# Optimization experiments

Measured on AMD Instinct MI355X. Metric: run time of the kernel, lower is better.

Reference implementation:

```python
import jax, jax.numpy as jnp
import numpy as np

LOCAL_MAX_DISP = 12
STRIDE = 1


def setup_inputs() -> dict:
    key = jax.random.key(0)
    k1, k2 = jax.random.split(key)
    B, H, W, C = 8, 256, 512, 32
    feat_l = jax.random.normal(k1, (B, H, W, C), dtype=jnp.float32)
    feat_r = jax.random.normal(k2, (B, H, W, C), dtype=jnp.float32)
    return {"feat_l": feat_l, "feat_r": feat_r}


def reference(feat_l, feat_r):
    # Faithful translation of CostVolume2D.call:
    # For disparity i = d*stride:
    #   cost[:, :, w, d] = sum_c |feat_l[:, :, w, c] - feat_r[:, :, w-i, c]|  for w >= i
    #   cost[:, :, w, d] = sum_c |feat_l[:, :, w, c]|                         for w <  i
    # The w < i case equals L1(feat_l - 0), so zero-padding feat_r on the left
    # by i columns reproduces both branches in one fused abs-diff reduction.
    B, H, W, C = feat_l.shape
    n_disp = LOCAL_MAX_DISP // STRIDE  # 12

    def cost_at(i):
        # shift feat_r right by i columns, zero-fill on the left  -> [B, H, W, C]
        shifted_r = jnp.pad(feat_r, ((0, 0), (0, 0), (i, 0), (0, 0)))[:, :, :W, :]
        return jnp.sum(jnp.abs(feat_l - shifted_r), axis=-1)  # [B, H, W]

    # small fixed loop over disparities (n_disp = 12), vectorized over B,H,W,C
    cost = jnp.stack([cost_at(d * STRIDE) for d in range(n_disp)], axis=-1)
    return cost  # [B, H, W, n_disp]
```

## Files before the change

### kernel.cpp

```cpp
#include <hip/hip_runtime.h>


constexpr int Wd   = 512;
constexpr int ND   = 12;
constexpr int NCOL = 272;

typedef float vfloat4 __attribute__((ext_vector_type(4)));

__device__ __forceinline__ float l1_4(float4 a, float4 b) {
    return fabsf(a.x - b.x) + fabsf(a.y - b.y) + fabsf(a.z - b.z) + fabsf(a.w - b.w);
}

__global__ __launch_bounds__(256) void cost_volume_kernel(
    const float* __restrict__ fl,
    const float* __restrict__ fr,
    float* __restrict__ out)
{
    __shared__ float4 lds4[4 * NCOL];

    const int t    = threadIdx.x;
    const int wave = t >> 6;
    const int lane = t & 63;
    const int wstart = (blockIdx.x & 1) * 256;
    const int bh     = blockIdx.x >> 1;
    const float* fr_row = fr + (size_t)bh * Wd * 32;

    const int w = wstart + t;
    const size_t pix = (size_t)bh * Wd + w;
    const float4* lp = reinterpret_cast<const float4*>(fl) + pix * 8;

    float res[ND];
    #pragma unroll
    for (int d = 0; d < ND; ++d) res[d] = 0.f;
    float lsum = 0.f;

    #pragma unroll
    for (int h = 0; h < 2; ++h) {
        if (h == 1) __syncthreads();

        #pragma unroll
        for (int run = 0; run < 5; ++run) {
            const int colr = run * 64 + lane;
            int col = wstart - 11 + colr;
            col = max(col, 0);
            if (run < 4 || lane < 267 - 256) {
                __builtin_amdgcn_global_load_lds(
                    (const __attribute__((address_space(1))) void*)(fr_row + (size_t)col * 32 + (h * 4 + wave) * 4),
                    (__attribute__((address_space(3))) void*)(lds4 + wave * NCOL + colr),
                    16, 0, 0);
            }
        }

        float4 L[4];
        #pragma unroll
        for (int ql = 0; ql < 4; ++ql) {
            L[ql] = lp[h * 4 + ql];
            lsum += fabsf(L[ql].x) + fabsf(L[ql].y) + fabsf(L[ql].z) + fabsf(L[ql].w);
        }

        __syncthreads();

        #pragma unroll
        for (int ql = 0; ql < 4; ++ql) {
            const float4 Lq = L[ql];
            const float4* base = &lds4[ql * NCOL + t];
            #pragma unroll
            for (int d = 0; d < ND; ++d) {
                res[d] += l1_4(Lq, base[11 - d]);
            }
        }
    }

    #pragma unroll
    for (int d = 0; d < ND; ++d)
        if (w < d) res[d] = lsum;

    vfloat4* op = reinterpret_cast<vfloat4*>(out + pix * ND);
    vfloat4 o0 = {res[0], res[1], res[2],  res[3]};
    vfloat4 o1 = {res[4], res[5], res[6],  res[7]};
    vfloat4 o2 = {res[8], res[9], res[10], res[11]};
    __builtin_nontemporal_store(o0, op + 0);
    __builtin_nontemporal_store(o1, op + 1);
    __builtin_nontemporal_store(o2, op + 2);
}

extern "C" void kernel_launch(void* const* d_in, const int* in_sizes, int n_in,
                              void* d_out, int out_size, void* d_ws, size_t ws_size,
                              hipStream_t stream)
{
    const float* fl = (const float*)d_in[0];
    const float* fr = (const float*)d_in[1];
    float* out = (float*)d_out;

    const int grid = 8 * 256 * 2;
    cost_volume_kernel<<<grid, 256, 0, stream>>>(fl, fr, out);
}
```

Baseline: 66.24 us.

## Compute two adjacent pixels per thread with double-buffered LDS staging over channel passes

Each block now covers a full image row and each thread computes two neighbouring pixels, so one LDS read of a right-feature vector serves disparities for both pixels (13 reads instead of 24 per channel group). Right features are staged into a double-buffered LDS ring with an even/odd interleaved slot layout across four channel passes, and the async load of the next pass overlaps compute on the current one. This is meant to cut LDS read traffic and hide global-load latency. In exchange it halves the grid and the number of waves, and raises register pressure with two accumulator sets.

Measured after the change: 190.7 us. 2.88x slower.

```diff
diff --git a/kernel.cpp b/kernel.cpp
--- a/kernel.cpp
+++ b/kernel.cpp
@@ -1,14 +1,18 @@
 #include <hip/hip_runtime.h>
 
 
-constexpr int Wd   = 512;
-constexpr int ND   = 12;
-constexpr int NCOL = 272;
+constexpr int Wd    = 512;
+constexpr int ND    = 12;
+constexpr int NSLOT = 576;
+constexpr int NPASS = 4;
 
 typedef float vfloat4 __attribute__((ext_vector_type(4)));
 
 __device__ __forceinline__ float l1_4(float4 a, float4 b) {
     return fabsf(a.x - b.x) + fabsf(a.y - b.y) + fabsf(a.z - b.z) + fabsf(a.w - b.w);
+}
+__device__ __forceinline__ float abs4(float4 a) {
+    return fabsf(a.x) + fabsf(a.y) + fabsf(a.z) + fabsf(a.w);
 }
 
 __global__ __launch_bounds__(256) void cost_volume_kernel(
@@ -16,72 +20,89 @@
     const float* __restrict__ fr,
     float* __restrict__ out)
 {
-    __shared__ float4 lds4[4 * NCOL];
+    __shared__ float4 lds4[2][2 * NSLOT];
 
     const int t    = threadIdx.x;
     const int wave = t >> 6;
     const int lane = t & 63;
-    const int wstart = (blockIdx.x & 1) * 256;
-    const int bh     = blockIdx.x >> 1;
+    const int bh   = blockIdx.x;
     const float* fr_row = fr + (size_t)bh * Wd * 32;
+    const size_t pix0 = (size_t)bh * Wd + 2 * t;
+    const float4* lp = reinterpret_cast<const float4*>(fl);
 
-    const int w = wstart + t;
-    const size_t pix = (size_t)bh * Wd + w;
-    const float4* lp = reinterpret_cast<const float4*>(fl) + pix * 8;
+    int basen[7];
+    #pragma unroll
+    for (int m = 0; m < 7; ++m) {
+        const int n = t + m;
+        basen[m] = ((n >> 5) << 6) + (n & 31);
+    }
 
-    float res[ND];
-    #pragma unroll
-    for (int d = 0; d < ND; ++d) res[d] = 0.f;
-    float lsum = 0.f;
-
-    #pragma unroll
-    for (int h = 0; h < 2; ++h) {
-        if (h == 1) __syncthreads();
-
+    auto stage = [&](int pp, int buf) {
         #pragma unroll
-        for (int run = 0; run < 5; ++run) {
-            const int colr = run * 64 + lane;
-            int col = wstart - 11 + colr;
-            col = max(col, 0);
-            if (run < 4 || lane < 267 - 256) {
+        for (int j = 0; j < 5; ++j) {
+            const int i = wave + 4 * j;
+            if (i < 18) {
+                const int k = i >> 1, q = i & 1;
+                int col = 64 * k + 2 * (lane & 31) + (lane >> 5) - 11;
+                col = min(max(col, 0), Wd - 1);
                 __builtin_amdgcn_global_load_lds(
-                    (const __attribute__((address_space(1))) void*)(fr_row + (size_t)col * 32 + (h * 4 + wave) * 4),
-                    (__attribute__((address_space(3))) void*)(lds4 + wave * NCOL + colr),
+                    (const __attribute__((address_space(1))) void*)(fr_row + (size_t)col * 32 + (pp * 2 + q) * 4),
+                    (__attribute__((address_space(3))) void*)(&lds4[buf][q * NSLOT + 64 * k + lane]),
                     16, 0, 0);
             }
         }
+    };
 
-        float4 L[4];
+    float res0[ND], res1[ND];
+    #pragma unroll
+    for (int d = 0; d < ND; ++d) { res0[d] = 0.f; res1[d] = 0.f; }
+    float lsum0 = 0.f, lsum1 = 0.f;
+
+    stage(0, 0);
+
+    #pragma unroll
+    for (int pp = 0; pp < NPASS; ++pp) {
+        __syncthreads();
+        if (pp + 1 < NPASS) stage(pp + 1, (pp + 1) & 1);
+
+        const int buf = pp & 1;
         #pragma unroll
-        for (int ql = 0; ql < 4; ++ql) {
-            L[ql] = lp[h * 4 + ql];
-            lsum += fabsf(L[ql].x) + fabsf(L[ql].y) + fabsf(L[ql].z) + fabsf(L[ql].w);
-        }
-
-        __syncthreads();
-
-        #pragma unroll
-        for (int ql = 0; ql < 4; ++ql) {
-            const float4 Lq = L[ql];
-            const float4* base = &lds4[ql * NCOL + t];
+        for (int q = 0; q < 2; ++q) {
+            const float4 A0 = lp[pix0 * 8 + pp * 2 + q];
+            const float4 A1 = lp[(pix0 + 1) * 8 + pp * 2 + q];
+            lsum0 += abs4(A0);
+            lsum1 += abs4(A1);
+            const float4* plane = &lds4[buf][q * NSLOT];
             #pragma unroll
-            for (int d = 0; d < ND; ++d) {
-                res[d] += l1_4(Lq, base[11 - d]);
+            for (int E = 0; E <= 12; ++E) {
+                const float4 rv = plane[basen[E >> 1] + 32 * (E & 1)];
+                if (E <= 11) res0[11 - E] += l1_4(A0, rv);
+                if (E >= 1)  res1[12 - E] += l1_4(A1, rv);
             }
         }
     }
 
-    #pragma unroll
-    for (int d = 0; d < ND; ++d)
-        if (w < d) res[d] = lsum;
+    if (t < 6) {
+        #pragma unroll
+        for (int d = 0; d < ND; ++d) {
+            if (d > 2 * t)     res0[d] = lsum0;
+            if (d > 2 * t + 1) res1[d] = lsum1;
+        }
+    }
 
-    vfloat4* op = reinterpret_cast<vfloat4*>(out + pix * ND);
-    vfloat4 o0 = {res[0], res[1], res[2],  res[3]};
-    vfloat4 o1 = {res[4], res[5], res[6],  res[7]};
-    vfloat4 o2 = {res[8], res[9], res[10], res[11]};
+    vfloat4* op = reinterpret_cast<vfloat4*>(out + pix0 * ND);
+    vfloat4 o0 = {res0[0], res0[1], res0[2],  res0[3]};
+    vfloat4 o1 = {res0[4], res0[5], res0[6],  res0[7]};
+    vfloat4 o2 = {res0[8], res0[9], res0[10], res0[11]};
+    vfloat4 o3 = {res1[0], res1[1], res1[2],  res1[3]};
+    vfloat4 o4 = {res1[4], res1[5], res1[6],  res1[7]};
+    vfloat4 o5 = {res1[8], res1[9], res1[10], res1[11]};
     __builtin_nontemporal_store(o0, op + 0);
     __builtin_nontemporal_store(o1, op + 1);
     __builtin_nontemporal_store(o2, op + 2);
+    __builtin_nontemporal_store(o3, op + 3);
+    __builtin_nontemporal_store(o4, op + 4);
+    __builtin_nontemporal_store(o5, op + 5);
 }
 
 extern "C" void kernel_launch(void* const* d_in, const int* in_sizes, int n_in,
@@ -92,6 +113,6 @@
     const float* fr = (const float*)d_in[1];
     float* out = (float*)d_out;
 
-    const int grid = 8 * 256 * 2;
+    const int grid = 8 * 256;
     cost_volume_kernel<<<grid, 256, 0, stream>>>(fl, fr, out);
 }
```
